# Kernel optimization log

Measured on AMD Instinct MI355X. Metric: run time of the kernel, lower is better.

## Reference

```python
import jax, jax.numpy as jnp
import numpy as np

N_NODES = 20000
N_EDGES = 320000
D = 128  # d_edge = d_node = d_global


def setup_inputs() -> dict:
    key = jax.random.key(0)
    ks = jax.random.split(key, 8)
    inv = lambda fan_in: 1.0 / np.sqrt(fan_in)
    return {
        "edge_attr": jax.random.normal(ks[0], (N_EDGES, D), dtype=jnp.float32),
        "node_attr": jax.random.normal(ks[1], (N_NODES, D), dtype=jnp.float32),
        "u": jax.random.normal(ks[2], (D,), dtype=jnp.float32),
        "senders": jax.random.randint(ks[3], (N_EDGES,), 0, N_NODES, dtype=jnp.int32),
        "receivers": jax.random.randint(ks[4], (N_EDGES,), 0, N_NODES, dtype=jnp.int32),
        "We": jax.random.normal(ks[5], (4 * D, D), dtype=jnp.float32) * inv(4 * D),
        "be": jnp.zeros((D,), dtype=jnp.float32),
        "Wv": jax.random.normal(ks[6], (3 * D, D), dtype=jnp.float32) * inv(3 * D),
        "bv": jnp.zeros((D,), dtype=jnp.float32),
        "Wu": jax.random.normal(ks[7], (3 * D, D), dtype=jnp.float32) * inv(3 * D),
        "bu": jnp.zeros((D,), dtype=jnp.float32),
    }


def reference(edge_attr, node_attr, u, senders, receivers, We, be, Wv, bv, Wu, bu):
    E = edge_attr.shape[0]
    N = node_attr.shape[0]
    u_e = jnp.broadcast_to(u, (E, u.shape[0]))
    u_v = jnp.broadcast_to(u, (N, u.shape[0]))

    # Edge block: phi_e(e, v_r, v_s, u) -- gather endpoint features per edge
    e_in = jnp.concatenate(
        [edge_attr, node_attr[receivers], node_attr[senders], u_e], axis=-1
    )  # [E, 4D]
    e_new = jax.nn.relu(e_in @ We + be)  # [E, D]

    # rho_ev: sum incoming edges per receiver node (scatter-add)
    aggr_e = jax.ops.segment_sum(e_new, receivers, num_segments=N)  # [N, D]

    # Node block: phi_v(aggr_e, v, u)
    v_in = jnp.concatenate([aggr_e, node_attr, u_v], axis=-1)  # [N, 3D]
    v_new = jax.nn.relu(v_in @ Wv + bv)  # [N, D]

    # Global block: rho_eu / rho_vu = mean, phi_u(aggr_e, aggr_v, u)
    aggr_e_u = jnp.mean(e_new, axis=0)
    aggr_v_u = jnp.mean(v_new, axis=0)
    u_in = jnp.concatenate([aggr_e_u, aggr_v_u, u], axis=-1)  # [3D]
    u_new = jax.nn.relu(u_in @ Wu + bu)  # [D]

    return e_new, v_new, u_new
```

## Files before the change

kernel.cpp:

```cpp
#include <hip/hip_runtime.h>
#include <hip/hip_bf16.h>


#define NN 20000
#define NE 320000
#define DD 128
#define SAS 136
#define SBS 136
#define NBLK 768
#define NTILE 5000

typedef unsigned short u16;
typedef __attribute__((ext_vector_type(8))) short bf16x8;
typedef __attribute__((ext_vector_type(4))) float f32x4;

__device__ __forceinline__ float b2f(unsigned short h) {
  return __uint_as_float(((unsigned int)h) << 16);
}
__device__ __forceinline__ unsigned short f2b(float f) {
  unsigned int u = __float_as_uint(f);
  unsigned int r = (u + 0x7fffu + ((u >> 16) & 1u)) >> 16;
  return (unsigned short)r;
}

__device__ __forceinline__ void mfma_core(const u16* sA, const u16* sBT,
                                          int lane, int w, f32x4 acc[4][2]) {
  int r15 = lane & 15;
  int koff = (lane >> 4) * 8;
#pragma unroll
  for (int k0 = 0; k0 < DD; k0 += 32) {
    bf16x8 a[4], b[2];
#pragma unroll
    for (int mt = 0; mt < 4; ++mt)
      a[mt] = *(const bf16x8*)&sA[(mt * 16 + r15) * SAS + k0 + koff];
#pragma unroll
    for (int nt = 0; nt < 2; ++nt)
      b[nt] = *(const bf16x8*)&sBT[(w * 32 + nt * 16 + r15) * SBS + k0 + koff];
#pragma unroll
    for (int mt = 0; mt < 4; ++mt)
#pragma unroll
      for (int nt = 0; nt < 2; ++nt)
        acc[mt][nt] = __builtin_amdgcn_mfma_f32_16x16x32_bf16(
            a[mt], b[nt], acc[mt][nt], 0, 0, 0);
  }
}

__device__ __forceinline__ void stage_w(u16* sBT, const u16* wsrc, int tid) {
  const uint4* ws = (const uint4*)wsrc;
  for (int i = tid; i < DD * DD / 8; i += 256) {
    int n = i >> 4, kk = (i & 15) * 8;
    *(uint4*)&sBT[n * SBS + kk] = ws[i];
  }
}

__global__ __launch_bounds__(256) void k_setup(const int* recv, int* counts,
                                               const float* We, const float* Wv,
                                               const float* u, const float* be,
                                               const float* bv, u16* wt,
                                               float* ce, float* cv) {
  __shared__ float su[DD];
  int b = blockIdx.x, tid = threadIdx.x;
  if (b < 1250) {
    atomicAdd(&counts[recv[b * 256 + tid]], 1);
  } else if (b < 1255) {
    int m = b - 1250;
    const float* W = (m == 0)   ? We
                     : (m == 1) ? We + 128 * DD
                     : (m == 2) ? We + 256 * DD
                     : (m == 3) ? Wv + 128 * DD
                                : Wv;
    u16* o = wt + (size_t)m * DD * DD;
    for (int i = tid; i < DD * DD; i += 256) {
      int k = i >> 7, n = i & 127;
      o[n * DD + k] = f2b(W[i]);
    }
  } else {
    if (tid < DD) su[tid] = u[tid];
    __syncthreads();
    if (tid < DD) {
      float a = be[tid], c = bv[tid];
      for (int k = 0; k < DD; ++k) {
        a = fmaf(su[k], We[(384 + k) * DD + tid], a);
        c = fmaf(su[k], Wv[(256 + k) * DD + tid], c);
      }
      ce[tid] = a;
      cv[tid] = c;
    }
  }
}

__global__ void k_scan(const int* counts, int* rowptr, int* cursor) {
  __shared__ int wsum[16];
  __shared__ int carry;
  int tid = threadIdx.x;
  int lane = tid & 63, wv = tid >> 6;
  if (tid == 0) carry = 0;
  __syncthreads();
  for (int base = 0; base < NN; base += 1024) {
    int i = base + tid;
    int v = (i < NN) ? counts[i] : 0;
    int x = v;
    for (int off = 1; off < 64; off <<= 1) {
      int t = __shfl_up(x, off);
      if (lane >= off) x += t;
    }
    if (lane == 63) wsum[wv] = x;
    __syncthreads();
    if (wv == 0 && lane < 16) {
      int y = wsum[lane];
      for (int off = 1; off < 16; off <<= 1) {
        int t = __shfl_up(y, off);
        if (lane >= off) y += t;
      }
      wsum[lane] = y;
    }
    __syncthreads();
    int woff = (wv > 0) ? wsum[wv - 1] : 0;
    int excl = carry + woff + (x - v);
    if (i < NN) {
      rowptr[i] = excl;
      cursor[i] = excl;
    }
    __syncthreads();
    if (tid == 0) carry += wsum[15];
    __syncthreads();
  }
  if (tid == 0) rowptr[NN] = carry;
}

__global__ __launch_bounds__(256) void k_mid(const int* recv, int* cursor,
                                             int* elist, const float* node_attr,
                                             const u16* wt, u16* P) {
  __shared__ __align__(16) u16 sA[64 * SAS];
  __shared__ __align__(16) u16 sBT[DD * SBS];
  int b = blockIdx.x, tid = threadIdx.x;
  if (b < 1250) {
    int e = b * 256 + tid;
    int slot = atomicAdd(&cursor[recv[e]], 1);
    elist[slot] = e;
    return;
  }
  int n0 = (b - 1250) * 64;
  for (int i = tid; i < 64 * DD / 4; i += 256) {
    int rr = i >> 5, cc = (i & 31) * 4;
    float4 a4 = (n0 + rr < NN)
                    ? ((const float4*)node_attr)[(size_t)(n0 + rr) * 32 + (i & 31)]
                    : make_float4(0, 0, 0, 0);
    ushort4 h;
    h.x = f2b(a4.x); h.y = f2b(a4.y); h.z = f2b(a4.z); h.w = f2b(a4.w);
    *(ushort4*)&sA[rr * SAS + cc] = h;
  }
  int lane = tid & 63, w = tid >> 6;
  int c15 = lane & 15, quad = lane >> 4;
  int col0 = w * 32 + c15, col1 = col0 + 16;
  for (int sel = 0; sel < 3; ++sel) {
    __syncthreads();
    stage_w(sBT, wt + (size_t)(1 + sel) * DD * DD, tid);
    __syncthreads();
    f32x4 acc[4][2] = {};
    mfma_core(sA, sBT, lane, w, acc);
#pragma unroll
    for (int mt = 0; mt < 4; ++mt)
#pragma unroll
      for (int r = 0; r < 4; ++r) {
        int n = n0 + mt * 16 + quad * 4 + r;
        if (n < NN) {
          u16* o = &P[(size_t)n * 384 + sel * 128];
          o[col0] = f2b(acc[mt][0][r]);
          o[col1] = f2b(acc[mt][1][r]);
        }
      }
  }
}

__global__ __launch_bounds__(256) void k_edge(const float* edge_attr,
                                              const u16* wt, const int* elist,
                                              const int* recv, const int* send,
                                              const u16* P, const float* ce,
                                              float* e_out, float* aggr,
                                              float* sum_e) {
  __shared__ __align__(16) u16 sBT[DD * SBS];
  __shared__ __align__(16) u16 sAO[64 * SAS];
  __shared__ int sEid[64], sRecv[64], sSend[64];
  int tid = threadIdx.x;
  int lane = tid & 63, w = tid >> 6;
  int r15 = lane & 15, quad = lane >> 4;
  int col0 = w * 32 + r15, col1 = col0 + 16;
  int myrow = tid >> 5;
  int mycol = (tid & 31) * 4;

  float4 areg[8];
  int eid8[8];
  int eidN = 0, rcN = 0, sdN = 0;
  int t = blockIdx.x;

  {
    int base = t * 64;
#pragma unroll
    for (int j = 0; j < 8; ++j) eid8[j] = elist[base + myrow + 8 * j];
    if (tid < 64) {
      eidN = elist[base + tid];
      rcN = recv[eidN];
      sdN = send[eidN];
    }
#pragma unroll
    for (int j = 0; j < 8; ++j)
      areg[j] = *(const float4*)&edge_attr[(size_t)eid8[j] * DD + mycol];
  }
  stage_w(sBT, wt, tid);
  float ce0 = ce[col0], ce1 = ce[col1];
  float colsum = 0.f;
  bool first = true;

  for (; t < NTILE; t += NBLK) {
    if (!first) __syncthreads();
    first = false;
#pragma unroll
    for (int j = 0; j < 8; ++j) {
      ushort4 h;
      h.x = f2b(areg[j].x); h.y = f2b(areg[j].y);
      h.z = f2b(areg[j].z); h.w = f2b(areg[j].w);
      *(ushort4*)&sAO[(myrow + 8 * j) * SAS + mycol] = h;
    }
    if (tid < 64) {
      sEid[tid] = eidN;
      sRecv[tid] = rcN;
      sSend[tid] = sdN;
    }
    __syncthreads();
    int tn = t + NBLK;
    if (tn < NTILE) {
      int base = tn * 64;
#pragma unroll
      for (int j = 0; j < 8; ++j) eid8[j] = elist[base + myrow + 8 * j];
      if (tid < 64) {
        eidN = elist[base + tid];
        rcN = recv[eidN];
        sdN = send[eidN];
      }
#pragma unroll
      for (int j = 0; j < 8; ++j)
        areg[j] = *(const float4*)&edge_attr[(size_t)eid8[j] * DD + mycol];
    }
    f32x4 acc[4][2] = {};
    mfma_core(sAO, sBT, lane, w, acc);
    float vv[4][2][4];
#pragma unroll
    for (int mt = 0; mt < 4; ++mt)
#pragma unroll
      for (int r = 0; r < 4; ++r) {
        int m = mt * 16 + quad * 4 + r;
        const u16* p1 = &P[(size_t)sRecv[m] * 384];
        const u16* p2 = &P[(size_t)sSend[m] * 384 + 128];
        vv[mt][0][r] =
            fmaxf(acc[mt][0][r] + b2f(p1[col0]) + b2f(p2[col0]) + ce0, 0.f);
        vv[mt][1][r] =
            fmaxf(acc[mt][1][r] + b2f(p1[col1]) + b2f(p2[col1]) + ce1, 0.f);
      }
    __syncthreads();
    u16* sOutH = sAO;
#pragma unroll
    for (int mt = 0; mt < 4; ++mt)
#pragma unroll
      for (int r = 0; r < 4; ++r) {
        int m = mt * 16 + quad * 4 + r;
        sOutH[m * SAS + col0] = f2b(vv[mt][0][r]);
        sOutH[m * SAS + col1] = f2b(vv[mt][1][r]);
      }
    __syncthreads();
    if (tid < DD) {
      float run = 0.f;
      int prev = sRecv[0];
      for (int r = 0; r < 64; ++r) {
        int cur = sRecv[r];
        float v = b2f(sOutH[r * SAS + tid]);
        if (cur != prev) {
          atomicAdd(&aggr[(size_t)prev * DD + tid], run);
          run = 0.f;
          prev = cur;
        }
        run += v;
        colsum += v;
      }
      atomicAdd(&aggr[(size_t)prev * DD + tid], run);
    } else {
      int tt = tid - 128;
#pragma unroll
      for (int j = 0; j < 8; ++j) {
        int i = tt + 128 * j;
        int row = i >> 4, ch = (i & 15) * 8;
        uint4 q = *(const uint4*)&sOutH[row * SAS + ch];
        float4 f0, f1;
        f0.x = b2f((u16)(q.x & 0xffff)); f0.y = b2f((u16)(q.x >> 16));
        f0.z = b2f((u16)(q.y & 0xffff)); f0.w = b2f((u16)(q.y >> 16));
        f1.x = b2f((u16)(q.z & 0xffff)); f1.y = b2f((u16)(q.z >> 16));
        f1.z = b2f((u16)(q.w & 0xffff)); f1.w = b2f((u16)(q.w >> 16));
        float* dst = &e_out[(size_t)sEid[row] * DD + ch];
        *(float4*)dst = f0;
        *(float4*)(dst + 4) = f1;
      }
    }
  }
  if (tid < DD) atomicAdd(&sum_e[tid], colsum);
}

__global__ __launch_bounds__(256) void k_node(const float* aggr, const u16* wt,
                                              const u16* P, const float* cv,
                                              float* v_out, float* sum_v) {
  __shared__ __align__(16) u16 sA[64 * SAS];
  __shared__ __align__(16) u16 sBT[DD * SBS];
  __shared__ float sCol[DD];
  int tid = threadIdx.x;
  int n0 = blockIdx.x * 64;
  stage_w(sBT, wt + (size_t)4 * DD * DD, tid);
  for (int i = tid; i < 64 * DD / 4; i += 256) {
    int rr = i >> 5, cc = (i & 31) * 4;
    float4 a4 = (n0 + rr < NN)
                    ? ((const float4*)aggr)[(size_t)(n0 + rr) * 32 + (i & 31)]
                    : make_float4(0, 0, 0, 0);
    ushort4 h;
    h.x = f2b(a4.x); h.y = f2b(a4.y); h.z = f2b(a4.z); h.w = f2b(a4.w);
    *(ushort4*)&sA[rr * SAS + cc] = h;
  }
  if (tid < DD) sCol[tid] = 0.f;
  __syncthreads();
  int lane = tid & 63, w = tid >> 6;
  f32x4 acc[4][2] = {};
  mfma_core(sA, sBT, lane, w, acc);
  int c15 = lane & 15, quad = lane >> 4;
  int col0 = w * 32 + c15, col1 = col0 + 16;
  float cv0 = cv[col0], cv1 = cv[col1];
  float cs0 = 0.f, cs1 = 0.f;
#pragma unroll
  for (int mt = 0; mt < 4; ++mt)
#pragma unroll
    for (int r = 0; r < 4; ++r) {
      int n = n0 + mt * 16 + quad * 4 + r;
      if (n < NN) {
        const u16* pv = &P[(size_t)n * 384 + 256];
        float v0 = fmaxf(acc[mt][0][r] + b2f(pv[col0]) + cv0, 0.f);
        float v1 = fmaxf(acc[mt][1][r] + b2f(pv[col1]) + cv1, 0.f);
        size_t ob = (size_t)n * DD;
        v_out[ob + col0] = v0;
        v_out[ob + col1] = v1;
        cs0 += v0;
        cs1 += v1;
      }
    }
  atomicAdd(&sCol[col0], cs0);
  atomicAdd(&sCol[col1], cs1);
  __syncthreads();
  if (tid < DD) atomicAdd(&sum_v[tid], sCol[tid]);
}

__global__ void k_global(const float* sumbuf, const float* u, const float* Wu,
                         const float* bu, float* out) {
  __shared__ float sin_[384];
  int j = threadIdx.x;
  sin_[j] = sumbuf[j] * (1.0f / (float)NE);
  sin_[128 + j] = sumbuf[128 + j] * (1.0f / (float)NN);
  sin_[256 + j] = u[j];
  __syncthreads();
  float a = bu[j];
  for (int k = 0; k < 384; ++k) a = fmaf(sin_[k], Wu[k * DD + j], a);
  out[j] = fmaxf(a, 0.f);
}

extern "C" void kernel_launch(void* const* d_in, const int* in_sizes, int n_in,
                              void* d_out, int out_size, void* d_ws,
                              size_t ws_size, hipStream_t stream) {
  const float* edge_attr = (const float*)d_in[0];
  const float* node_attr = (const float*)d_in[1];
  const float* u = (const float*)d_in[2];
  const int* senders = (const int*)d_in[3];
  const int* receivers = (const int*)d_in[4];
  const float* We = (const float*)d_in[5];
  const float* be = (const float*)d_in[6];
  const float* Wv = (const float*)d_in[7];
  const float* bv = (const float*)d_in[8];
  const float* Wu = (const float*)d_in[9];
  const float* bu = (const float*)d_in[10];

  float* e_out = (float*)d_out;
  float* v_out = e_out + (size_t)NE * DD;
  float* u_out = v_out + (size_t)NN * DD;

  int* counts = (int*)d_ws;
  float* sumbuf = (float*)d_ws + NN;
  float* aggr = (float*)d_ws + NN + 256;
  int* rowptr = (int*)d_ws + NN + 256 + NN * DD;
  int* cursor = rowptr + NN + 1;
  int* elist = cursor + NN;
  size_t off = (size_t)(NN + 256 + NN * DD + (NN + 1) + NN + NE);
  off = (off + 3) & ~(size_t)3;
  u16* wt = (u16*)((float*)d_ws + off);
  u16* P = wt + (size_t)5 * DD * DD;
  float* ce = (float*)(P + (size_t)NN * 384);
  float* cv = ce + 128;

  hipMemsetAsync(d_ws, 0, (size_t)(NN + 256 + NN * DD) * 4, stream);
  k_setup<<<1256, 256, 0, stream>>>(receivers, counts, We, Wv, u, be, bv, wt,
                                    ce, cv);
  k_scan<<<1, 1024, 0, stream>>>(counts, rowptr, cursor);
  k_mid<<<1250 + 313, 256, 0, stream>>>(receivers, cursor, elist, node_attr,
                                        wt, P);
  k_edge<<<NBLK, 256, 0, stream>>>(edge_attr, wt, elist, receivers, senders, P,
                                   ce, e_out, aggr, sumbuf);
  k_node<<<(NN + 63) / 64, 256, 0, stream>>>(aggr, wt, P, cv, v_out,
                                             sumbuf + 128);
  k_global<<<1, 128, 0, stream>>>(sumbuf, u, Wu, bu, u_out);
}
```

Measured before the change: 518.1 us.

## Restructure edge kernel: 512 threads, register-resident weights, staged P gathers in LDS

The edge kernel moves to 512-thread blocks (8 waves), each wave owning 16 output columns. Each wave keeps its slice of the edge weight matrix in registers instead of staging the full matrix in shared memory. The per-edge receiver and sender projections of P are now fetched as coalesced 16-byte loads into shared buffers while the MFMA runs, replacing scattered 2-byte global reads in the epilogue. The scatter-add is split across two thread halves and the grid drops from 768 to 512 blocks, at the cost of more registers per thread and extra barriers.

```diff
diff --git a/kernel.cpp b/kernel.cpp
--- a/kernel.cpp
+++ b/kernel.cpp
@@ -7,7 +7,7 @@
 #define DD 128
 #define SAS 136
 #define SBS 136
-#define NBLK 768
+#define NBLK 512
 #define NTILE 5000
 
 typedef unsigned short u16;
@@ -173,42 +173,49 @@
   }
 }
 
-__global__ __launch_bounds__(256) void k_edge(const float* edge_attr,
-                                              const u16* wt, const int* elist,
-                                              const int* recv, const int* send,
-                                              const u16* P, const float* ce,
-                                              float* e_out, float* aggr,
-                                              float* sum_e) {
-  __shared__ __align__(16) u16 sBT[DD * SBS];
-  __shared__ __align__(16) u16 sAO[64 * SAS];
+__global__ __launch_bounds__(512, 4) void k_edge(const float* edge_attr,
+                                                 const u16* wt, const int* elist,
+                                                 const int* recv, const int* send,
+                                                 const u16* P, const float* ce,
+                                                 float* e_out, float* aggr,
+                                                 float* sum_e) {
+  __shared__ __align__(16) u16 sA[64 * SAS];
+  __shared__ __align__(16) u16 sPr[64 * SAS];
+  __shared__ __align__(16) u16 sPs[64 * SAS];
   __shared__ int sEid[64], sRecv[64], sSend[64];
   int tid = threadIdx.x;
   int lane = tid & 63, w = tid >> 6;
   int r15 = lane & 15, quad = lane >> 4;
-  int col0 = w * 32 + r15, col1 = col0 + 16;
+  int koff = quad * 8;
+  int col0 = w * 16 + r15;
   int myrow = tid >> 5;
   int mycol = (tid & 31) * 4;
 
-  float4 areg[8];
-  int eid8[8];
+  bf16x8 breg[4];
+#pragma unroll
+  for (int kk = 0; kk < 4; ++kk)
+    breg[kk] =
+        *(const bf16x8*)&wt[(size_t)(w * 16 + r15) * DD + kk * 32 + koff];
+  float ce0 = ce[col0];
+
+  float4 areg[4];
+  int eid4[4];
   int eidN = 0, rcN = 0, sdN = 0;
   int t = blockIdx.x;
 
   {
     int base = t * 64;
 #pragma unroll
-    for (int j = 0; j < 8; ++j) eid8[j] = elist[base + myrow + 8 * j];
+    for (int j = 0; j < 4; ++j) eid4[j] = elist[base + myrow + 16 * j];
     if (tid < 64) {
       eidN = elist[base + tid];
       rcN = recv[eidN];
       sdN = send[eidN];
     }
 #pragma unroll
-    for (int j = 0; j < 8; ++j)
-      areg[j] = *(const float4*)&edge_attr[(size_t)eid8[j] * DD + mycol];
-  }
-  stage_w(sBT, wt, tid);
-  float ce0 = ce[col0], ce1 = ce[col1];
+    for (int j = 0; j < 4; ++j)
+      areg[j] = *(const float4*)&edge_attr[(size_t)eid4[j] * DD + mycol];
+  }
   float colsum = 0.f;
   bool first = true;
 
@@ -216,11 +223,11 @@
     if (!first) __syncthreads();
     first = false;
 #pragma unroll
-    for (int j = 0; j < 8; ++j) {
+    for (int j = 0; j < 4; ++j) {
       ushort4 h;
       h.x = f2b(areg[j].x); h.y = f2b(areg[j].y);
       h.z = f2b(areg[j].z); h.w = f2b(areg[j].w);
-      *(ushort4*)&sAO[(myrow + 8 * j) * SAS + mycol] = h;
+      *(ushort4*)&sA[(myrow + 16 * j) * SAS + mycol] = h;
     }
     if (tid < 64) {
       sEid[tid] = eidN;
@@ -228,80 +235,103 @@
       sSend[tid] = sdN;
     }
     __syncthreads();
+
+    uint4 q[4];
+    int pr_[4], pc_[4], ph_[4];
+#pragma unroll
+    for (int j = 0; j < 4; ++j) {
+      int idx = tid + 512 * j;
+      int half = idx >> 10;
+      int ii = idx & 1023;
+      int row = ii >> 4, ch = ii & 15;
+      const uint4* src =
+          (half == 0) ? (const uint4*)&P[(size_t)sRecv[row] * 384] + ch
+                      : (const uint4*)&P[(size_t)sSend[row] * 384 + 128] + ch;
+      q[j] = *src;
+      pr_[j] = row; pc_[j] = ch; ph_[j] = half;
+    }
     int tn = t + NBLK;
     if (tn < NTILE) {
       int base = tn * 64;
 #pragma unroll
-      for (int j = 0; j < 8; ++j) eid8[j] = elist[base + myrow + 8 * j];
+      for (int j = 0; j < 4; ++j) eid4[j] = elist[base + myrow + 16 * j];
       if (tid < 64) {
         eidN = elist[base + tid];
         rcN = recv[eidN];
         sdN = send[eidN];
       }
 #pragma unroll
-      for (int j = 0; j < 8; ++j)
-        areg[j] = *(const float4*)&edge_attr[(size_t)eid8[j] * DD + mycol];
-    }
-    f32x4 acc[4][2] = {};
-    mfma_core(sAO, sBT, lane, w, acc);
-    float vv[4][2][4];
+      for (int j = 0; j < 4; ++j)
+        areg[j] = *(const float4*)&edge_attr[(size_t)eid4[j] * DD + mycol];
+    }
+
+    f32x4 acc[4] = {};
+#pragma unroll
+    for (int kk = 0; kk < 4; ++kk) {
+      bf16x8 a[4];
+#pragma unroll
+      for (int mt = 0; mt < 4; ++mt)
+        a[mt] = *(const bf16x8*)&sA[(mt * 16 + r15) * SAS + kk * 32 + koff];
+#pragma unroll
+      for (int mt = 0; mt < 4; ++mt)
+        acc[mt] = __builtin_amdgcn_mfma_f32_16x16x32_bf16(a[mt], breg[kk],
+                                                          acc[mt], 0, 0, 0);
+    }
+#pragma unroll
+    for (int j = 0; j < 4; ++j) {
+      u16* dst = (ph_[j] == 0) ? sPr : sPs;
+      *(uint4*)&dst[pr_[j] * SAS + pc_[j] * 8] = q[j];
+    }
+    __syncthreads();
+
 #pragma unroll
     for (int mt = 0; mt < 4; ++mt)
 #pragma unroll
       for (int r = 0; r < 4; ++r) {
         int m = mt * 16 + quad * 4 + r;
-        const u16* p1 = &P[(size_t)sRecv[m] * 384];
-        const u16* p2 = &P[(size_t)sSend[m] * 384 + 128];
-        vv[mt][0][r] =
-            fmaxf(acc[mt][0][r] + b2f(p1[col0]) + b2f(p2[col0]) + ce0, 0.f);
-        vv[mt][1][r] =
-            fmaxf(acc[mt][1][r] + b2f(p1[col1]) + b2f(p2[col1]) + ce1, 0.f);
-      }
-    __syncthreads();
-    u16* sOutH = sAO;
-#pragma unroll
-    for (int mt = 0; mt < 4; ++mt)
-#pragma unroll
-      for (int r = 0; r < 4; ++r) {
-        int m = mt * 16 + quad * 4 + r;
-        sOutH[m * SAS + col0] = f2b(vv[mt][0][r]);
-        sOutH[m * SAS + col1] = f2b(vv[mt][1][r]);
-      }
-    __syncthreads();
-    if (tid < DD) {
+        float v = fmaxf(acc[mt][r] + b2f(sPr[m * SAS + col0]) +
+                            b2f(sPs[m * SAS + col0]) + ce0,
+                        0.f);
+        sA[m * SAS + col0] = f2b(v);
+      }
+    __syncthreads();
+
+    if (tid < 256) {
+      int col = tid & 127, half = tid >> 7;
+      int r0 = half * 32;
       float run = 0.f;
-      int prev = sRecv[0];
-      for (int r = 0; r < 64; ++r) {
+      int prev = sRecv[r0];
+      for (int r = r0; r < r0 + 32; ++r) {
         int cur = sRecv[r];
-        float v = b2f(sOutH[r * SAS + tid]);
+        float v = b2f(sA[r * SAS + col]);
         if (cur != prev) {
-          atomicAdd(&aggr[(size_t)prev * DD + tid], run);
+          atomicAdd(&aggr[(size_t)prev * DD + col], run);
           run = 0.f;
           prev = cur;
         }
         run += v;
         colsum += v;
       }
-      atomicAdd(&aggr[(size_t)prev * DD + tid], run);
+      atomicAdd(&aggr[(size_t)prev * DD + col], run);
     } else {
-      int tt = tid - 128;
-#pragma unroll
-      for (int j = 0; j < 8; ++j) {
-        int i = tt + 128 * j;
+      int tt = tid - 256;
+#pragma unroll
+      for (int j = 0; j < 4; ++j) {
+        int i = tt + 256 * j;
         int row = i >> 4, ch = (i & 15) * 8;
-        uint4 q = *(const uint4*)&sOutH[row * SAS + ch];
+        uint4 qq = *(const uint4*)&sA[row * SAS + ch];
         float4 f0, f1;
-        f0.x = b2f((u16)(q.x & 0xffff)); f0.y = b2f((u16)(q.x >> 16));
-        f0.z = b2f((u16)(q.y & 0xffff)); f0.w = b2f((u16)(q.y >> 16));
-        f1.x = b2f((u16)(q.z & 0xffff)); f1.y = b2f((u16)(q.z >> 16));
-        f1.z = b2f((u16)(q.w & 0xffff)); f1.w = b2f((u16)(q.w >> 16));
+        f0.x = b2f((u16)(qq.x & 0xffff)); f0.y = b2f((u16)(qq.x >> 16));
+        f0.z = b2f((u16)(qq.y & 0xffff)); f0.w = b2f((u16)(qq.y >> 16));
+        f1.x = b2f((u16)(qq.z & 0xffff)); f1.y = b2f((u16)(qq.z >> 16));
+        f1.z = b2f((u16)(qq.w & 0xffff)); f1.w = b2f((u16)(qq.w >> 16));
         float* dst = &e_out[(size_t)sEid[row] * DD + ch];
         *(float4*)dst = f0;
         *(float4*)(dst + 4) = f1;
       }
     }
   }
-  if (tid < DD) atomicAdd(&sum_e[tid], colsum);
+  if (tid < 256) atomicAdd(&sum_e[tid & 127], colsum);
 }
 
 __global__ __launch_bounds__(256) void k_node(const float* aggr, const u16* wt,
@@ -404,7 +434,7 @@
   k_scan<<<1, 1024, 0, stream>>>(counts, rowptr, cursor);
   k_mid<<<1250 + 313, 256, 0, stream>>>(receivers, cursor, elist, node_attr,
                                         wt, P);
-  k_edge<<<NBLK, 256, 0, stream>>>(edge_attr, wt, elist, receivers, senders, P,
+  k_edge<<<NBLK, 512, 0, stream>>>(edge_attr, wt, elist, receivers, senders, P,
                                    ce, e_out, aggr, sumbuf);
   k_node<<<(NN + 63) / 64, 256, 0, stream>>>(aggr, wt, P, cv, v_out,
                                              sumbuf + 128);
```

After: 490.2 us. 1.06x faster.
